# Kernel tuning notes

Measured on AMD Instinct MI355X. Metric: run time of the kernel, lower is better.

## Reference

```python
import jax, jax.numpy as jnp
import numpy as np

B = 2          # batch size
T2 = 9         # temporal groups (b*t2 = grid_sample batch)
T3 = 27        # t1 // t2
T1 = 243       # t2 * t3
P = 17         # joints
K2 = 9         # kernel_size ** 2
C = 128        # dim_img
CH = [48, 96, 192, 384]
HW = [(96, 72), (48, 36), (24, 18), (12, 9)]
ALPHA = 0.9


def setup_inputs() -> dict:
    key = jax.random.key(0)
    ks = jax.random.split(key, 16)
    inp = {}
    N = B * T2
    for i, (c, (h, w)) in enumerate(zip(CH, HW)):
        inp[f"f{i}"] = jax.random.normal(ks[i], (N, c, h, w), jnp.float32)
    inp["query"] = jax.random.normal(ks[4], (B, T1, P * K2, C), jnp.float32)
    # key holds normalized grid coords in [-1, 1]
    inp["key"] = jax.random.uniform(ks[5], (N, T3, P * K2, 2), jnp.float32) * 2.0 - 1.0
    inp["value"] = jax.random.normal(ks[6], (B, T1, P, C), jnp.float32)
    s = 0.05
    inp["w_off"] = jax.random.normal(ks[7], (2, C), jnp.float32) * s
    inp["b_off"] = jnp.zeros((2,), jnp.float32)
    inp["w_attn"] = jax.random.normal(ks[8], (2, C), jnp.float32) * s
    inp["b_attn"] = jnp.zeros((2,), jnp.float32)
    for i, c in enumerate(CH):
        inp[f"we{i}"] = jax.random.normal(ks[9 + i], (C, c), jnp.float32) * s
        inp[f"be{i}"] = jnp.zeros((C,), jnp.float32)
    inp["conv_w"] = jax.random.normal(ks[13], (C, C, K2), jnp.float32) * s
    inp["conv_b"] = jnp.zeros((C,), jnp.float32)
    return inp


def _grid_sample(img, grid):
    """Bilinear grid_sample, align_corners=False, zero padding.
    img: [N, C, H, W]; grid: [N, Hg, Wg, 2] in [-1,1] (x=width, y=height).
    Returns [N, Hg, Wg, C] (channels-last for the following 1x1 conv)."""
    N, Cin, H, W = img.shape
    gx, gy = grid[..., 0], grid[..., 1]
    ix = ((gx + 1.0) * W - 1.0) * 0.5
    iy = ((gy + 1.0) * H - 1.0) * 0.5
    ix0 = jnp.floor(ix); iy0 = jnp.floor(iy)
    wx1 = ix - ix0; wx0 = 1.0 - wx1
    wy1 = iy - iy0; wy0 = 1.0 - wy1
    bidx = jnp.arange(N)[:, None, None]

    def gather(yy, xx):
        yi = yy.astype(jnp.int32); xi = xx.astype(jnp.int32)
        valid = (yi >= 0) & (yi < H) & (xi >= 0) & (xi < W)
        yc = jnp.clip(yi, 0, H - 1); xc = jnp.clip(xi, 0, W - 1)
        v = img[bidx, :, yc, xc]  # [N, Hg, Wg, C]
        return v * valid[..., None].astype(img.dtype)

    out = (gather(iy0, ix0) * (wy0 * wx0)[..., None]
           + gather(iy0, ix0 + 1.0) * (wy0 * wx1)[..., None]
           + gather(iy0 + 1.0, ix0) * (wy1 * wx0)[..., None]
           + gather(iy0 + 1.0, ix0 + 1.0) * (wy1 * wx1)[..., None])
    return out


def reference(f0, f1, f2, f3, query, key, value,
              w_off, b_off, w_attn, b_attn,
              we0, be0, we1, be1, we2, be2, we3, be3,
              conv_w, conv_b):
    b, t1, p, c = value.shape            # [B, 243, 17, 128]
    t3 = key.shape[1]                    # 27
    t2 = t1 // t3                        # 9

    # learned offsets per query location, squashed by tanh
    off = jnp.tanh(jnp.einsum('btqc,oc->btqo', query, w_off) + b_off)   # [b,t1,153,2]
    # per-joint softmax weights, tiled over the k^2 kernel taps
    aw = jax.nn.softmax(jnp.einsum('btpc,oc->btpo', value, w_attn) + b_attn, axis=-1)  # [b,t1,17,2]
    aw = jnp.tile(aw, (1, 1, K2, 1))                                     # [b,t1,153,2]

    sp = (off * aw).reshape(b * t2, t3, p * K2, 2)
    sampling_positions = key + sp                                        # [b*t2, 27, 153, 2]

    fmaps = (f0, f1, f2, f3)
    ws = (we0, we1, we2, we3)
    bs = (be0, be1, be2, be3)
    feats = []
    for f, w, bb in zip(fmaps, ws, bs):
        g = _grid_sample(f, sampling_positions)                          # [b*t2, 27, 153, C_in]
        e = jnp.einsum('nhwc,oc->nhwo', g, w) + bb                        # 1x1 conv embed -> 128
        feats.append(e.reshape(b, t2 * t3, p * K2, C))                    # [b, 243, 153, 128]
    new_query = jnp.mean(jnp.stack(feats, axis=-2), axis=-2)             # fuse 4 levels
    new_query = (1.0 - ALPHA) * new_query + ALPHA * query

    # grouped-by-position conv1d over the k^2 taps (full-width kernel -> length 1)
    x = new_query.reshape(b, t1, p, K2, c)                               # 'b t (p k) c'
    new_value = jnp.einsum('btpkc,ock->btpo', x, conv_w) + conv_b        # [b, 243, 17, 128]
    return (new_query, new_value, sampling_positions)
```

## Files before the change

### kernel.cpp

```cpp
#include <hip/hip_runtime.h>
#include <hip/hip_bf16.h>

static constexpr int NQ_SIZE = 9517824;
static constexpr int NV_SIZE = 1057536;
static constexpr int NPOS    = 74358;
static constexpr int M_CONV  = 8262;

static constexpr long E0_OFF = 0;
static constexpr long E1_OFF = 15925248;
static constexpr long E2_OFF = E1_OFF + 3981312;
static constexpr long E3_OFF = E2_OFF + 995328;
static constexpr long E_END  = E3_OFF + 248832;

static constexpr int SEG_L3 = 18;
static constexpr int SEG_SP = SEG_L3 + 486;
static constexpr int SEG_L2 = SEG_SP + 72;
static constexpr int SEG_L1 = SEG_L2 + 252;
static constexpr int SEG_L0 = SEG_L1 + 972;
static constexpr int SEG_CT = SEG_L0 + 576;
static constexpr int PREP_GRID = SEG_CT;

typedef __attribute__((ext_vector_type(8))) short short8;
typedef __attribute__((ext_vector_type(4))) float floatx4;

__device__ __forceinline__ float bf2f(unsigned short u) {
    union { unsigned int i; float f; } v; v.i = ((unsigned)u) << 16; return v.f;
}
__device__ __forceinline__ unsigned short f2bf_rne(float f) {
    union { float f; unsigned int i; } v; v.f = f;
    unsigned int u = v.i;
    u += 0x7fffu + ((u >> 16) & 1u);
    return (unsigned short)(u >> 16);
}
__device__ __forceinline__ short8 pack8(const float* t) {
    union { unsigned short u[8]; short8 s; } r;
    #pragma unroll
    for (int i = 0; i < 8; ++i) r.u[i] = f2bf_rne(t[i]);
    return r.s;
}

template<int K, int M, bool FULLM>
__device__ __forceinline__ void proj_body(
    const float* __restrict__ A, const float* __restrict__ W,
    unsigned short* __restrict__ Eo, int m0, int tid,
    unsigned short (*Bs)[104])
{
    constexpr int KC      = (K < 96) ? K : 96;
    constexpr int KCPAD   = (KC + 31) & ~31;
    constexpr int KT      = KCPAD / 32;
    constexpr int NCH     = K / KC;
    constexpr bool NEEDPAD = (KCPAD != KC);

    const int lane = tid & 63;
    const int wave = tid >> 6;
    const int l15  = lane & 15;
    const int quad = lane >> 4;
    const int mg0  = m0 + wave * 32 + l15;
    const int mg1  = mg0 + 16;
    const bool v0  = FULLM || (mg0 < M);
    const bool v1  = FULLM || (mg1 < M);

    floatx4 acc[2][8];
    #pragma unroll
    for (int f = 0; f < 2; ++f)
        #pragma unroll
        for (int nt = 0; nt < 8; ++nt) acc[f][nt] = (floatx4){0.f, 0.f, 0.f, 0.f};

    const int so  = tid >> 1;
    const int skb = (tid & 1) * (KCPAD / 2);

    #pragma unroll 1
    for (int ch = 0; ch < NCH; ++ch) {
        const int kc = ch * KC;
        if (ch) __syncthreads();
        {
            const float* wp = W + (long)so * K + kc + skb;
            #pragma unroll
            for (int k = 0; k < KCPAD / 2; k += 8) {
                float t[8];
                #pragma unroll
                for (int j = 0; j < 8; ++j)
                    t[j] = (!NEEDPAD || (skb + k + j < KC)) ? wp[k + j] : 0.f;
                unsigned short u[8];
                #pragma unroll
                for (int j = 0; j < 8; ++j) u[j] = f2bf_rne(t[j]);
                *(uint4*)&Bs[so][skb + k] = *(const uint4*)u;
            }
        }
        __syncthreads();

        #pragma unroll
        for (int kt = 0; kt < KT; ++kt) {
            const int kg = kc + kt * 32 + quad * 8;
            float a0[8], a1[8];
            const float* ap = A + (long)kg * M + mg0;
            const bool fastk = !NEEDPAD || (kg + 8 <= K);
            if (FULLM && fastk) {
                #pragma unroll
                for (int j = 0; j < 8; ++j) {
                    a0[j] = ap[(long)j * M];
                    a1[j] = ap[(long)j * M + 16];
                }
            } else {
                #pragma unroll
                for (int j = 0; j < 8; ++j) {
                    a0[j] = 0.f; a1[j] = 0.f;
                    if (kg + j < K) {
                        if (v0) a0[j] = ap[(long)j * M];
                        if (v1) a1[j] = ap[(long)j * M + 16];
                    }
                }
            }
            short8 af0 = pack8(a0);
            short8 af1 = pack8(a1);
            #pragma unroll
            for (int nt = 0; nt < 8; ++nt) {
                short8 bf = *(const short8*)&Bs[nt * 16 + l15][kt * 32 + quad * 8];
                acc[0][nt] = __builtin_amdgcn_mfma_f32_16x16x32_bf16(af0, bf, acc[0][nt], 0, 0, 0);
                acc[1][nt] = __builtin_amdgcn_mfma_f32_16x16x32_bf16(af1, bf, acc[1][nt], 0, 0, 0);
            }
        }
    }

    #pragma unroll
    for (int f = 0; f < 2; ++f) {
        const int rb = m0 + wave * 32 + f * 16 + quad * 4;
        #pragma unroll
        for (int nt = 0; nt < 8; ++nt) {
            const int col = nt * 16 + l15;
            #pragma unroll
            for (int r = 0; r < 4; ++r) {
                if (FULLM || (rb + r < M))
                    Eo[(long)(rb + r) * 128 + col] = f2bf_rne(acc[f][nt][r]);
            }
        }
    }
}

__global__ __launch_bounds__(256) void prep_k(
    const float* __restrict__ f0, const float* __restrict__ f1,
    const float* __restrict__ f2, const float* __restrict__ f3,
    const float* __restrict__ we0, const float* __restrict__ we1,
    const float* __restrict__ we2, const float* __restrict__ we3,
    const float* __restrict__ conv_w, unsigned short* __restrict__ convT2,
    const float* __restrict__ query, const float* __restrict__ value,
    const float* __restrict__ key,
    const float* __restrict__ w_off, const float* __restrict__ b_off,
    const float* __restrict__ w_attn, const float* __restrict__ b_attn,
    float* __restrict__ samp, unsigned short* __restrict__ Ebase)
{
    const int bid = blockIdx.x;
    const int tid = threadIdx.x;

    if (bid < SEG_L3 || (bid >= SEG_SP && bid < SEG_L0)) {
        __shared__ unsigned short Bs[128][104];

        if (bid < SEG_L3) {
            int n = bid;
            proj_body<384, 108, false>(f3 + (long)n * 384 * 108, we3,
                Ebase + E3_OFF + (long)n * 108 * 128, 0, tid, Bs);
        } else if (bid < SEG_L2) {
            int r = bid - SEG_SP; int n = r >> 2, t = r & 3;
            const float* A = f2 + (long)n * 192 * 432;
            unsigned short* Eo = Ebase + E2_OFF + (long)n * 432 * 128;
            if (t < 3) proj_body<192, 432, true >(A, we2, Eo, t * 128, tid, Bs);
            else       proj_body<192, 432, false>(A, we2, Eo, t * 128, tid, Bs);
        } else if (bid < SEG_L1) {
            int r = bid - SEG_L2; int n = r / 14, t = r - n * 14;
            const float* A = f1 + (long)n * 96 * 1728;
            unsigned short* Eo = Ebase + E1_OFF + (long)n * 1728 * 128;
            if (t < 13) proj_body<96, 1728, true >(A, we1, Eo, t * 128, tid, Bs);
            else        proj_body<96, 1728, false>(A, we1, Eo, t * 128, tid, Bs);
        } else {
            int r = bid - SEG_L1; int n = r / 54, t = r - n * 54;
            proj_body<48, 6912, true>(f0 + (long)n * 48 * 6912, we0,
                Ebase + E0_OFF + (long)n * 6912 * 128, t * 128, tid, Bs);
        }
    } else if (bid < SEG_SP) {
        const int bt1 = bid - SEG_L3;
        const int b  = bt1 / 243, t1 = bt1 - b * 243;
        const int t2 = t1 / 27,  t3 = t1 - t2 * 27;
        const int n  = b * 9 + t2;
        __shared__ float logit[17][2];
        __shared__ float aw[17][2];

        if (tid < 34) {
            int p = tid >> 1, o = tid & 1;
            const float* vrow = value + ((long)bt1 * 17 + p) * 128;
            const float* wrow = w_attn + o * 128;
            float s = 0.f;
            for (int c = 0; c < 128; c += 4) {
                float4 v = *(const float4*)(vrow + c);
                float4 w = *(const float4*)(wrow + c);
                s += v.x * w.x + v.y * w.y + v.z * w.z + v.w * w.w;
            }
            logit[p][o] = s + b_attn[o];
        }
        __syncthreads();
        if (tid < 17) {
            float l0 = logit[tid][0], l1 = logit[tid][1];
            float mx = fmaxf(l0, l1);
            float e0 = expf(l0 - mx), e1 = expf(l1 - mx);
            float inv = 1.f / (e0 + e1);
            aw[tid][0] = e0 * inv; aw[tid][1] = e1 * inv;
        }
        __syncthreads();
        for (int j = tid; j < 306; j += 256) {
            int q = j >> 1, o = j & 1;
            const float* qrow = query + ((long)bt1 * 153 + q) * 128;
            const float* wrow = w_off + o * 128;
            float s = 0.f;
            for (int c = 0; c < 128; c += 4) {
                float4 v = *(const float4*)(qrow + c);
                float4 w = *(const float4*)(wrow + c);
                s += v.x * w.x + v.y * w.y + v.z * w.z + v.w * w.w;
            }
            float off = tanhf(s + b_off[o]);
            float sp = off * aw[q % 17][o];
            long kidx = (((long)n * 27 + t3) * 153 + q) * 2 + o;
            samp[kidx] = key[kidx] + sp;
        }
    } else {
        int idx = (bid - SEG_L0) * 256 + tid;
        if (idx < 147456) {
            int o = idx / 1152, kk = idx - o * 1152;
            int k2 = kk >> 7, c = kk & 127;
            convT2[idx] = f2bf_rne(conv_w[o * 1152 + c * 9 + k2]);
        }
    }
}

__global__ __launch_bounds__(256) void gather_k(
    const unsigned short* __restrict__ Ebase,
    const float* __restrict__ samp, const float* __restrict__ query,
    const float* __restrict__ be0, const float* __restrict__ be1,
    const float* __restrict__ be2, const float* __restrict__ be3,
    float* __restrict__ nq)
{
    const int tid = threadIdx.x;
    const int pos = blockIdx.x * 8 + (tid >> 5);
    if (pos >= NPOS) return;
    const int c4 = (tid & 31) << 2;
    const int bt1 = pos / 153, q = pos - bt1 * 153;
    const int b  = bt1 / 243, t1 = bt1 - b * 243;
    const int t2 = t1 / 27,  t3 = t1 - t2 * 27;
    const int n  = b * 9 + t2;
    const long sbase = (((long)n * 27 + t3) * 153 + q) * 2;
    const float gx = samp[sbase], gy = samp[sbase + 1];

    float ax = 0.f, ay = 0.f, az = 0.f, aww = 0.f;
    const long Eoffs[4] = {E0_OFF, E1_OFF, E2_OFF, E3_OFF};
    const int Hs[4] = {96, 48, 24, 12}, Wd[4] = {72, 36, 18, 9};
    #pragma unroll
    for (int l = 0; l < 4; ++l) {
        const int H = Hs[l], W = Wd[l];
        const unsigned short* E = Ebase + Eoffs[l] + (long)n * H * W * 128 + c4;
        float ix = ((gx + 1.f) * (float)W - 1.f) * 0.5f;
        float iy = ((gy + 1.f) * (float)H - 1.f) * 0.5f;
        float fx0 = floorf(ix), fy0 = floorf(iy);
        int x0 = (int)fx0, y0 = (int)fy0;
        int x1 = x0 + 1, y1 = y0 + 1;
        float wx1 = ix - fx0, wx0 = 1.f - wx1;
        float wy1 = iy - fy0, wy0 = 1.f - wy1;
        float w00 = wy0 * wx0, w01 = wy0 * wx1, w10 = wy1 * wx0, w11 = wy1 * wx1;
        bool vy0 = (unsigned)y0 < (unsigned)H, vy1 = (unsigned)y1 < (unsigned)H;
        bool vx0 = (unsigned)x0 < (unsigned)W, vx1 = (unsigned)x1 < (unsigned)W;
        if (vy0 && vx0) { ushort4 v = *(const ushort4*)(E + ((long)y0 * W + x0) * 128);
            ax = fmaf(w00, bf2f(v.x), ax); ay = fmaf(w00, bf2f(v.y), ay);
            az = fmaf(w00, bf2f(v.z), az); aww = fmaf(w00, bf2f(v.w), aww); }
        if (vy0 && vx1) { ushort4 v = *(const ushort4*)(E + ((long)y0 * W + x1) * 128);
            ax = fmaf(w01, bf2f(v.x), ax); ay = fmaf(w01, bf2f(v.y), ay);
            az = fmaf(w01, bf2f(v.z), az); aww = fmaf(w01, bf2f(v.w), aww); }
        if (vy1 && vx0) { ushort4 v = *(const ushort4*)(E + ((long)y1 * W + x0) * 128);
            ax = fmaf(w10, bf2f(v.x), ax); ay = fmaf(w10, bf2f(v.y), ay);
            az = fmaf(w10, bf2f(v.z), az); aww = fmaf(w10, bf2f(v.w), aww); }
        if (vy1 && vx1) { ushort4 v = *(const ushort4*)(E + ((long)y1 * W + x1) * 128);
            ax = fmaf(w11, bf2f(v.x), ax); ay = fmaf(w11, bf2f(v.y), ay);
            az = fmaf(w11, bf2f(v.z), az); aww = fmaf(w11, bf2f(v.w), aww); }
    }
    float bsx = be0[c4]     + be1[c4]     + be2[c4]     + be3[c4];
    float bsy = be0[c4 + 1] + be1[c4 + 1] + be2[c4 + 1] + be3[c4 + 1];
    float bsz = be0[c4 + 2] + be1[c4 + 2] + be2[c4 + 2] + be3[c4 + 2];
    float bsw = be0[c4 + 3] + be1[c4 + 3] + be2[c4 + 3] + be3[c4 + 3];
    float mx = 0.25f * (ax + bsx), my = 0.25f * (ay + bsy);
    float mz = 0.25f * (az + bsz), mw = 0.25f * (aww + bsw);
    const long qi = ((long)bt1 * 153 + q) * 128 + c4;
    float4 qv = *(const float4*)(query + qi);
    float4 o;
    o.x = 0.1f * mx + 0.9f * qv.x;
    o.y = 0.1f * my + 0.9f * qv.y;
    o.z = 0.1f * mz + 0.9f * qv.z;
    o.w = 0.1f * mw + 0.9f * qv.w;
    *(float4*)(nq + qi) = o;
}

__global__ __launch_bounds__(256) void conv_mfma_k(
    const float* __restrict__ nq, const unsigned short* __restrict__ convT2,
    const float* __restrict__ conv_b, float* __restrict__ nv)
{
    __shared__ unsigned short As[32][40];
    __shared__ unsigned short Bs[64][40];

    const int tid  = threadIdx.x;
    const int lane = tid & 63;
    const int wave = tid >> 6;
    const int wm = (wave & 1) * 16;
    const int wn = (wave >> 1) * 32;
    const int m0 = blockIdx.x * 32;
    const int n0 = blockIdx.y * 64;
    const int l15  = lane & 15;
    const int quad = lane >> 4;

    floatx4 acc[2];
    acc[0] = (floatx4){0.f, 0.f, 0.f, 0.f};
    acc[1] = acc[0];

    const int am = tid >> 3;
    const int ak = (tid & 7) << 2;
    const int bn = tid >> 2;
    const int bk = (tid & 3) << 3;

    float4 a0; uint4 bv;
    auto fetch = [&](int k0) {
        a0 = (float4){0,0,0,0};
        int row = m0 + am;
        if (row < M_CONV)
            a0 = *(const float4*)(nq + (long)row * 1152 + k0 + ak);
        bv = *(const uint4*)(convT2 + (long)(n0 + bn) * 1152 + k0 + bk);
    };
    fetch(0);

    for (int k0 = 0; k0 < 1152; k0 += 32) {
        unsigned short t[4] = {f2bf_rne(a0.x), f2bf_rne(a0.y), f2bf_rne(a0.z), f2bf_rne(a0.w)};
        *(uint2*)&As[am][ak] = *(const uint2*)t;
        *(uint4*)&Bs[bn][bk] = bv;
        __syncthreads();
        if (k0 + 32 < 1152) fetch(k0 + 32);

        short8 af = *(const short8*)&As[wm + l15][quad * 8];
        #pragma unroll
        for (int nt = 0; nt < 2; ++nt) {
            short8 bf = *(const short8*)&Bs[wn + nt * 16 + l15][quad * 8];
            acc[nt] = __builtin_amdgcn_mfma_f32_16x16x32_bf16(af, bf, acc[nt], 0, 0, 0);
        }
        __syncthreads();
    }

    #pragma unroll
    for (int nt = 0; nt < 2; ++nt) {
        int col = n0 + wn + nt * 16 + l15;
        float bias = conv_b[col];
        #pragma unroll
        for (int r = 0; r < 4; ++r) {
            int row = m0 + wm + quad * 4 + r;
            if (row < M_CONV)
                nv[(long)row * 128 + col] = acc[nt][r] + bias;
        }
    }
}

extern "C" void kernel_launch(void* const* d_in, const int* in_sizes, int n_in,
                              void* d_out, int out_size, void* d_ws, size_t ws_size,
                              hipStream_t stream) {
    const float* f0     = (const float*)d_in[0];
    const float* f1     = (const float*)d_in[1];
    const float* f2     = (const float*)d_in[2];
    const float* f3     = (const float*)d_in[3];
    const float* query  = (const float*)d_in[4];
    const float* key    = (const float*)d_in[5];
    const float* value  = (const float*)d_in[6];
    const float* w_off  = (const float*)d_in[7];
    const float* b_off  = (const float*)d_in[8];
    const float* w_attn = (const float*)d_in[9];
    const float* b_attn = (const float*)d_in[10];
    const float* we0    = (const float*)d_in[11];
    const float* be0    = (const float*)d_in[12];
    const float* we1    = (const float*)d_in[13];
    const float* be1    = (const float*)d_in[14];
    const float* we2    = (const float*)d_in[15];
    const float* be2    = (const float*)d_in[16];
    const float* we3    = (const float*)d_in[17];
    const float* be3    = (const float*)d_in[18];
    const float* conv_w = (const float*)d_in[19];
    const float* conv_b = (const float*)d_in[20];

    float* out  = (float*)d_out;
    float* nq   = out;
    float* nv   = out + NQ_SIZE;
    float* samp = out + NQ_SIZE + NV_SIZE;

    unsigned short* Ebase  = (unsigned short*)d_ws;
    unsigned short* convT2 = Ebase + E_END;

    prep_k<<<PREP_GRID, 256, 0, stream>>>(
        f0, f1, f2, f3, we0, we1, we2, we3, conv_w, convT2,
        query, value, key, w_off, b_off, w_attn, b_attn, samp, Ebase);

    gather_k<<<(NPOS + 7) / 8, 256, 0, stream>>>(Ebase, samp, query, be0, be1, be2, be3, nq);

    conv_mfma_k<<<dim3(259, 2), 256, 0, stream>>>(nq, convT2, conv_b, nv);
}
```

Before: 240.7 us.

## Fuse sampling-offset computation into gather kernel and deepen conv/proj pipelining

The per-(b,t1) sampling-position blocks in prep are replaced by a small attention-weight softmax segment that writes into the new_value output buffer as scratch. The query-offset dot product, tanh and key addition move into gather_k, so the query row is read once there and samp is no longer written and re-read. The projection body now issues all global loads for a chunk before the barrier to overlap latency, and the conv GEMM uses a K step of 64 instead of 32, halving barriers. Costs are more register pressure in proj_body and reuse of nv as scratch before conv overwrites it.

```diff
diff --git a/kernel.cpp b/kernel.cpp
--- a/kernel.cpp
+++ b/kernel.cpp
@@ -12,9 +12,9 @@
 static constexpr long E3_OFF = E2_OFF + 995328;
 static constexpr long E_END  = E3_OFF + 248832;
 
-static constexpr int SEG_L3 = 18;
-static constexpr int SEG_SP = SEG_L3 + 486;
-static constexpr int SEG_L2 = SEG_SP + 72;
+static constexpr int SEG_AW = 65;
+static constexpr int SEG_L3 = SEG_AW + 18;
+static constexpr int SEG_L2 = SEG_L3 + 72;
 static constexpr int SEG_L1 = SEG_L2 + 252;
 static constexpr int SEG_L0 = SEG_L1 + 972;
 static constexpr int SEG_CT = SEG_L0 + 576;
@@ -72,47 +72,56 @@
     #pragma unroll 1
     for (int ch = 0; ch < NCH; ++ch) {
         const int kc = ch * KC;
-        if (ch) __syncthreads();
+
+        float bt[KCPAD / 2];
         {
             const float* wp = W + (long)so * K + kc + skb;
             #pragma unroll
-            for (int k = 0; k < KCPAD / 2; k += 8) {
-                float t[8];
-                #pragma unroll
-                for (int j = 0; j < 8; ++j)
-                    t[j] = (!NEEDPAD || (skb + k + j < KC)) ? wp[k + j] : 0.f;
-                unsigned short u[8];
-                #pragma unroll
-                for (int j = 0; j < 8; ++j) u[j] = f2bf_rne(t[j]);
-                *(uint4*)&Bs[so][skb + k] = *(const uint4*)u;
-            }
-        }
-        __syncthreads();
-
+            for (int j = 0; j < KCPAD / 2; ++j) {
+                bt[j] = 0.f;
+                if (!NEEDPAD || (skb + j < KC)) bt[j] = wp[j];
+            }
+        }
+
+        float a0[KT][8], a1[KT][8];
         #pragma unroll
         for (int kt = 0; kt < KT; ++kt) {
             const int kg = kc + kt * 32 + quad * 8;
-            float a0[8], a1[8];
             const float* ap = A + (long)kg * M + mg0;
-            const bool fastk = !NEEDPAD || (kg + 8 <= K);
-            if (FULLM && fastk) {
+            if (FULLM && (!NEEDPAD || (kg + 8 <= K))) {
                 #pragma unroll
                 for (int j = 0; j < 8; ++j) {
-                    a0[j] = ap[(long)j * M];
-                    a1[j] = ap[(long)j * M + 16];
+                    a0[kt][j] = ap[(long)j * M];
+                    a1[kt][j] = ap[(long)j * M + 16];
                 }
             } else {
                 #pragma unroll
                 for (int j = 0; j < 8; ++j) {
-                    a0[j] = 0.f; a1[j] = 0.f;
+                    a0[kt][j] = 0.f; a1[kt][j] = 0.f;
                     if (kg + j < K) {
-                        if (v0) a0[j] = ap[(long)j * M];
-                        if (v1) a1[j] = ap[(long)j * M + 16];
+                        if (v0) a0[kt][j] = ap[(long)j * M];
+                        if (v1) a1[kt][j] = ap[(long)j * M + 16];
                     }
                 }
             }
-            short8 af0 = pack8(a0);
-            short8 af1 = pack8(a1);
+        }
+
+        if (ch) __syncthreads();
+        {
+            #pragma unroll
+            for (int j = 0; j < KCPAD / 2; j += 8) {
+                unsigned short u[8];
+                #pragma unroll
+                for (int i = 0; i < 8; ++i) u[i] = f2bf_rne(bt[j + i]);
+                *(uint4*)&Bs[so][skb + j] = *(const uint4*)u;
+            }
+        }
+        __syncthreads();
+
+        #pragma unroll
+        for (int kt = 0; kt < KT; ++kt) {
+            short8 af0 = pack8(a0[kt]);
+            short8 af1 = pack8(a1[kt]);
             #pragma unroll
             for (int nt = 0; nt < 8; ++nt) {
                 short8 bf = *(const short8*)&Bs[nt * 16 + l15][kt * 32 + quad * 8];
@@ -143,24 +152,40 @@
     const float* __restrict__ we0, const float* __restrict__ we1,
     const float* __restrict__ we2, const float* __restrict__ we3,
     const float* __restrict__ conv_w, unsigned short* __restrict__ convT2,
-    const float* __restrict__ query, const float* __restrict__ value,
-    const float* __restrict__ key,
-    const float* __restrict__ w_off, const float* __restrict__ b_off,
+    const float* __restrict__ value,
     const float* __restrict__ w_attn, const float* __restrict__ b_attn,
-    float* __restrict__ samp, unsigned short* __restrict__ Ebase)
+    float* __restrict__ awbuf, unsigned short* __restrict__ Ebase)
 {
     const int bid = blockIdx.x;
     const int tid = threadIdx.x;
 
-    if (bid < SEG_L3 || (bid >= SEG_SP && bid < SEG_L0)) {
+    if (bid < SEG_AW) {
+        int t = bid * 256 + tid;
+        if (t < 16524) {
+            int rp = t >> 1, o = t & 1;
+            const float* vrow = value + (long)rp * 128;
+            const float* wrow = w_attn + o * 128;
+            float s = 0.f;
+            for (int c = 0; c < 128; c += 4) {
+                float4 v = *(const float4*)(vrow + c);
+                float4 w = *(const float4*)(wrow + c);
+                s += v.x * w.x + v.y * w.y + v.z * w.z + v.w * w.w;
+            }
+            s += b_attn[o];
+            float so = __shfl_xor(s, 1);
+            float m = fmaxf(s, so);
+            float e = __expf(s - m), eo = __expf(so - m);
+            awbuf[t] = e / (e + eo);
+        }
+    } else if (bid < SEG_L0) {
         __shared__ unsigned short Bs[128][104];
 
         if (bid < SEG_L3) {
-            int n = bid;
+            int n = bid - SEG_AW;
             proj_body<384, 108, false>(f3 + (long)n * 384 * 108, we3,
                 Ebase + E3_OFF + (long)n * 108 * 128, 0, tid, Bs);
         } else if (bid < SEG_L2) {
-            int r = bid - SEG_SP; int n = r >> 2, t = r & 3;
+            int r = bid - SEG_L3; int n = r >> 2, t = r & 3;
             const float* A = f2 + (long)n * 192 * 432;
             unsigned short* Eo = Ebase + E2_OFF + (long)n * 432 * 128;
             if (t < 3) proj_body<192, 432, true >(A, we2, Eo, t * 128, tid, Bs);
@@ -176,50 +201,6 @@
             proj_body<48, 6912, true>(f0 + (long)n * 48 * 6912, we0,
                 Ebase + E0_OFF + (long)n * 6912 * 128, t * 128, tid, Bs);
         }
-    } else if (bid < SEG_SP) {
-        const int bt1 = bid - SEG_L3;
-        const int b  = bt1 / 243, t1 = bt1 - b * 243;
-        const int t2 = t1 / 27,  t3 = t1 - t2 * 27;
-        const int n  = b * 9 + t2;
-        __shared__ float logit[17][2];
-        __shared__ float aw[17][2];
-
-        if (tid < 34) {
-            int p = tid >> 1, o = tid & 1;
-            const float* vrow = value + ((long)bt1 * 17 + p) * 128;
-            const float* wrow = w_attn + o * 128;
-            float s = 0.f;
-            for (int c = 0; c < 128; c += 4) {
-                float4 v = *(const float4*)(vrow + c);
-                float4 w = *(const float4*)(wrow + c);
-                s += v.x * w.x + v.y * w.y + v.z * w.z + v.w * w.w;
-            }
-            logit[p][o] = s + b_attn[o];
-        }
-        __syncthreads();
-        if (tid < 17) {
-            float l0 = logit[tid][0], l1 = logit[tid][1];
-            float mx = fmaxf(l0, l1);
-            float e0 = expf(l0 - mx), e1 = expf(l1 - mx);
-            float inv = 1.f / (e0 + e1);
-            aw[tid][0] = e0 * inv; aw[tid][1] = e1 * inv;
-        }
-        __syncthreads();
-        for (int j = tid; j < 306; j += 256) {
-            int q = j >> 1, o = j & 1;
-            const float* qrow = query + ((long)bt1 * 153 + q) * 128;
-            const float* wrow = w_off + o * 128;
-            float s = 0.f;
-            for (int c = 0; c < 128; c += 4) {
-                float4 v = *(const float4*)(qrow + c);
-                float4 w = *(const float4*)(wrow + c);
-                s += v.x * w.x + v.y * w.y + v.z * w.z + v.w * w.w;
-            }
-            float off = tanhf(s + b_off[o]);
-            float sp = off * aw[q % 17][o];
-            long kidx = (((long)n * 27 + t3) * 153 + q) * 2 + o;
-            samp[kidx] = key[kidx] + sp;
-        }
     } else {
         int idx = (bid - SEG_L0) * 256 + tid;
         if (idx < 147456) {
@@ -232,21 +213,47 @@
 
 __global__ __launch_bounds__(256) void gather_k(
     const unsigned short* __restrict__ Ebase,
-    const float* __restrict__ samp, const float* __restrict__ query,
+    const float* __restrict__ query, const float* __restrict__ key,
+    const float* __restrict__ w_off, const float* __restrict__ b_off,
+    const float* __restrict__ awbuf,
     const float* __restrict__ be0, const float* __restrict__ be1,
     const float* __restrict__ be2, const float* __restrict__ be3,
-    float* __restrict__ nq)
+    float* __restrict__ nq, float* __restrict__ samp)
 {
     const int tid = threadIdx.x;
     const int pos = blockIdx.x * 8 + (tid >> 5);
     if (pos >= NPOS) return;
-    const int c4 = (tid & 31) << 2;
+    const int l32 = tid & 31;
+    const int c4  = l32 << 2;
     const int bt1 = pos / 153, q = pos - bt1 * 153;
     const int b  = bt1 / 243, t1 = bt1 - b * 243;
     const int t2 = t1 / 27,  t3 = t1 - t2 * 27;
     const int n  = b * 9 + t2;
-    const long sbase = (((long)n * 27 + t3) * 153 + q) * 2;
-    const float gx = samp[sbase], gy = samp[sbase + 1];
+    const int p  = q % 17;
+
+    const long qi = ((long)bt1 * 153 + q) * 128 + c4;
+    const float4 qv = *(const float4*)(query + qi);
+
+    float4 w0 = *(const float4*)(w_off + c4);
+    float4 w1 = *(const float4*)(w_off + 128 + c4);
+    float s0 = qv.x * w0.x + qv.y * w0.y + qv.z * w0.z + qv.w * w0.w;
+    float s1 = qv.x * w1.x + qv.y * w1.y + qv.z * w1.z + qv.w * w1.w;
+    #pragma unroll
+    for (int m = 16; m >= 1; m >>= 1) {
+        s0 += __shfl_xor(s0, m);
+        s1 += __shfl_xor(s1, m);
+    }
+    const float aw0 = awbuf[(bt1 * 17 + p) * 2];
+    const float aw1 = awbuf[(bt1 * 17 + p) * 2 + 1];
+    const float off0 = tanhf(s0 + b_off[0]);
+    const float off1 = tanhf(s1 + b_off[1]);
+    const long kidx = (((long)n * 27 + t3) * 153 + q) * 2;
+    const float gx = key[kidx]     + off0 * aw0;
+    const float gy = key[kidx + 1] + off1 * aw1;
+    if (l32 == 0) {
+        samp[kidx]     = gx;
+        samp[kidx + 1] = gy;
+    }
 
     float ax = 0.f, ay = 0.f, az = 0.f, aww = 0.f;
     const long Eoffs[4] = {E0_OFF, E1_OFF, E2_OFF, E3_OFF};
@@ -284,8 +291,6 @@
     float bsw = be0[c4 + 3] + be1[c4 + 3] + be2[c4 + 3] + be3[c4 + 3];
     float mx = 0.25f * (ax + bsx), my = 0.25f * (ay + bsy);
     float mz = 0.25f * (az + bsz), mw = 0.25f * (aww + bsw);
-    const long qi = ((long)bt1 * 153 + q) * 128 + c4;
-    float4 qv = *(const float4*)(query + qi);
     float4 o;
     o.x = 0.1f * mx + 0.9f * qv.x;
     o.y = 0.1f * my + 0.9f * qv.y;
@@ -298,8 +303,8 @@
     const float* __restrict__ nq, const unsigned short* __restrict__ convT2,
     const float* __restrict__ conv_b, float* __restrict__ nv)
 {
-    __shared__ unsigned short As[32][40];
-    __shared__ unsigned short Bs[64][40];
+    __shared__ unsigned short As[32][72];
+    __shared__ unsigned short Bs[64][72];
 
     const int tid  = threadIdx.x;
     const int lane = tid & 63;
@@ -316,32 +321,40 @@
     acc[1] = acc[0];
 
     const int am = tid >> 3;
-    const int ak = (tid & 7) << 2;
+    const int ak = (tid & 7) << 3;
     const int bn = tid >> 2;
-    const int bk = (tid & 3) << 3;
-
-    float4 a0; uint4 bv;
+    const int bk = (tid & 3) << 4;
+
+    float4 a0, a1; uint4 bv0, bv1;
     auto fetch = [&](int k0) {
-        a0 = (float4){0,0,0,0};
+        a0 = (float4){0,0,0,0}; a1 = a0;
         int row = m0 + am;
-        if (row < M_CONV)
+        if (row < M_CONV) {
             a0 = *(const float4*)(nq + (long)row * 1152 + k0 + ak);
-        bv = *(const uint4*)(convT2 + (long)(n0 + bn) * 1152 + k0 + bk);
+            a1 = *(const float4*)(nq + (long)row * 1152 + k0 + ak + 4);
+        }
+        bv0 = *(const uint4*)(convT2 + (long)(n0 + bn) * 1152 + k0 + bk);
+        bv1 = *(const uint4*)(convT2 + (long)(n0 + bn) * 1152 + k0 + bk + 8);
     };
     fetch(0);
 
-    for (int k0 = 0; k0 < 1152; k0 += 32) {
-        unsigned short t[4] = {f2bf_rne(a0.x), f2bf_rne(a0.y), f2bf_rne(a0.z), f2bf_rne(a0.w)};
-        *(uint2*)&As[am][ak] = *(const uint2*)t;
-        *(uint4*)&Bs[bn][bk] = bv;
+    for (int k0 = 0; k0 < 1152; k0 += 64) {
+        unsigned short t[8] = {f2bf_rne(a0.x), f2bf_rne(a0.y), f2bf_rne(a0.z), f2bf_rne(a0.w),
+                               f2bf_rne(a1.x), f2bf_rne(a1.y), f2bf_rne(a1.z), f2bf_rne(a1.w)};
+        *(uint4*)&As[am][ak] = *(const uint4*)t;
+        *(uint4*)&Bs[bn][bk] = bv0;
+        *(uint4*)&Bs[bn][bk + 8] = bv1;
         __syncthreads();
-        if (k0 + 32 < 1152) fetch(k0 + 32);
-
-        short8 af = *(const short8*)&As[wm + l15][quad * 8];
-        #pragma unroll
-        for (int nt = 0; nt < 2; ++nt) {
-            short8 bf = *(const short8*)&Bs[wn + nt * 16 + l15][quad * 8];
-            acc[nt] = __builtin_amdgcn_mfma_f32_16x16x32_bf16(af, bf, acc[nt], 0, 0, 0);
+        if (k0 + 64 < 1152) fetch(k0 + 64);
+
+        #pragma unroll
+        for (int kt = 0; kt < 2; ++kt) {
+            short8 af = *(const short8*)&As[wm + l15][kt * 32 + quad * 8];
+            #pragma unroll
+            for (int nt = 0; nt < 2; ++nt) {
+                short8 bf = *(const short8*)&Bs[wn + nt * 16 + l15][kt * 32 + quad * 8];
+                acc[nt] = __builtin_amdgcn_mfma_f32_16x16x32_bf16(af, bf, acc[nt], 0, 0, 0);
+            }
         }
         __syncthreads();
     }
@@ -391,12 +404,14 @@
 
     unsigned short* Ebase  = (unsigned short*)d_ws;
     unsigned short* convT2 = Ebase + E_END;
+    float* awbuf = nv;
 
     prep_k<<<PREP_GRID, 256, 0, stream>>>(
         f0, f1, f2, f3, we0, we1, we2, we3, conv_w, convT2,
-        query, value, key, w_off, b_off, w_attn, b_attn, samp, Ebase);
-
-    gather_k<<<(NPOS + 7) / 8, 256, 0, stream>>>(Ebase, samp, query, be0, be1, be2, be3, nq);
+        value, w_attn, b_attn, awbuf, Ebase);
+
+    gather_k<<<(NPOS + 7) / 8, 256, 0, stream>>>(
+        Ebase, query, key, w_off, b_off, awbuf, be0, be1, be2, be3, nq, samp);
 
     conv_mfma_k<<<dim3(259, 2), 256, 0, stream>>>(nq, convT2, conv_b, nv);
 }
```

Result: faster. 232.8 us (-3.3%).
